# Performance work log

Hardware: AMD Instinct MI355X
Metric: run time of the kernel (lower is better)

The kernel has to match this reference:

```python
import jax, jax.numpy as jnp
import numpy as np

HEADS = 8
DIM = 64      # dim
DH = 64       # dim_head
DK = 24       # dim_k (== dim_head_k * heads, required by reshape in forward)
DHK = 3       # dim_head_k (also conv groups)


def setup_inputs() -> dict:
    key = jax.random.key(0)
    ks = jax.random.split(key, 10)
    b, h, w = 4, 128, 128
    return {
        "x_in": jax.random.normal(ks[0], (b, h, w, DIM), jnp.float32),
        "illu_fea_trans": jax.random.normal(ks[1], (b, h, w, DIM), jnp.float32),
        "illu_map_trans": jax.random.normal(ks[2], (b, h, w, DK), jnp.float32),
        # Linear weights stored as [in, out] (torch stores [out, in]; math y = x @ W_in_out)
        "Wq": jax.random.normal(ks[3], (DIM, HEADS * DH), jnp.float32) * 0.05,
        "Wk": jax.random.normal(ks[4], (DK, HEADS * DHK), jnp.float32) * 0.05,
        "Wv": jax.random.normal(ks[5], (DIM, HEADS * DH), jnp.float32) * 0.05,
        "rescale": jnp.ones((HEADS, 1, 1), jnp.float32),
        "Wp": jax.random.normal(ks[6], (HEADS * DHK, DK), jnp.float32) * 0.05,
        "bp": jax.random.normal(ks[7], (DK,), jnp.float32) * 0.05,
        # grouped conv weights, OIHW: [out=24, in/groups=8, 3, 3]
        "conv1_w": jax.random.normal(ks[8], (DK, DK // DHK, 3, 3), jnp.float32) * 0.05,
        "conv2_w": jax.random.normal(ks[9], (DK, DK // DHK, 3, 3), jnp.float32) * 0.05,
    }


def _gconv(x_nchw, w_oihw):
    return jax.lax.conv_general_dilated(
        x_nchw, w_oihw, window_strides=(1, 1), padding='SAME',
        feature_group_count=DHK,
        dimension_numbers=('NCHW', 'OIHW', 'NCHW'))


def reference(x_in, illu_fea_trans, illu_map_trans, Wq, Wk, Wv, rescale, Wp, bp, conv1_w, conv2_w):
    b, h, w, c = x_in.shape
    n = h * w
    # projections
    q = (x_in.reshape(b, n, c) @ Wq).reshape(b, n, HEADS, DH)
    k_inp = illu_map_trans.reshape(b, n, DK) @ Wk            # [b, n, heads*dhk]
    v = (illu_fea_trans.reshape(b, n, c) @ Wv).reshape(b, n, HEADS, DH)
    kh = k_inp.reshape(b, n, HEADS, DHK)
    q = q / (DIM ** 0.5)  # note: scaled by sqrt(dim), not sqrt(dim_head)
    # channel-wise cross-attention: attn over channel dims, contracting tokens n
    attn = jnp.einsum('bnhk,bnhd->bhkd', kh, q) * rescale[None]  # [b, heads, dhk, dh]
    attn = jax.nn.softmax(attn, axis=-1)
    out = jnp.einsum('bhkd,bnhd->bnkh', attn, v)             # [b, n, dhk, heads]
    out = out.reshape(b, n, DHK * HEADS) @ Wp + bp           # proj
    out = out.reshape(b, h, w, DK)
    # positional branch: two grouped 3x3 convs with exact GELU on k_inp
    kx = k_inp.reshape(b, h, w, DK).transpose(0, 3, 1, 2)    # NCHW
    y = _gconv(kx, conv1_w)
    y = jax.nn.gelu(y, approximate=False)
    y = _gconv(y, conv2_w)
    return out + y.transpose(0, 2, 3, 1)
```

## Files before the change

### kernel.cpp

```cpp
#include <hip/hip_runtime.h>
#include <math.h>

#define HEADS 8
#define DIM   64
#define DK    24
#define DHK   3
#define BB    4
#define HH    128
#define WW    128
#define NN    (HH*WW)
#define QSCALE 0.125f

__global__ __launch_bounds__(256) void s_reduce(
    const float* __restrict__ imap,
    const float* __restrict__ x,
    float* __restrict__ Sp_part)
{
    __shared__ float part[4*1536];
    const int tid = threadIdx.x;
    const int blk = blockIdx.x;
    const int b = blk >> 6, chunk = blk & 63;
    const int w = tid >> 6, lane = tid & 63;
    const int cq = lane & 15;
    const int ig = lane >> 4;

    const long tok0 = (long)b * NN + chunk * 256 + w * 64;
    const float* xp = x    + tok0 * 64 + cq * 4;
    const float* mp = imap + tok0 * 24 + ig * 6;

    float acc[6][4];
    #pragma unroll
    for (int r = 0; r < 6; ++r)
        #pragma unroll
        for (int q = 0; q < 4; ++q) acc[r][q] = 0.f;

    for (int t = 0; t < 64; ++t) {
        float4 xv = *(const float4*)(xp + t * 64);
        float2 m0 = *(const float2*)(mp + t * 24);
        float2 m1 = *(const float2*)(mp + t * 24 + 2);
        float2 m2 = *(const float2*)(mp + t * 24 + 4);
        float mm[6] = {m0.x, m0.y, m1.x, m1.y, m2.x, m2.y};
        #pragma unroll
        for (int r = 0; r < 6; ++r) {
            acc[r][0] += mm[r] * xv.x;
            acc[r][1] += mm[r] * xv.y;
            acc[r][2] += mm[r] * xv.z;
            acc[r][3] += mm[r] * xv.w;
        }
    }

    float* pp = part + w * 1536;
    #pragma unroll
    for (int r = 0; r < 6; ++r) {
        float4 v = {acc[r][0], acc[r][1], acc[r][2], acc[r][3]};
        *(float4*)(pp + (ig * 6 + r) * 64 + cq * 4) = v;
    }
    __syncthreads();

    for (int e = tid; e < 1536; e += 256)
        Sp_part[(long)blk * 1536 + e] =
            part[e] + part[1536 + e] + part[3072 + e] + part[4608 + e];
}

__global__ __launch_bounds__(256) void attn_fused(
    const float* __restrict__ Sp_part,
    const float* __restrict__ Wk,
    const float* __restrict__ Wq,
    const float* __restrict__ Wv,
    const float* __restrict__ rescale,
    const float* __restrict__ Wp,
    float* __restrict__ Pt)
{
    __shared__ float Sp_l[1536];
    __shared__ float S_l[1536];
    __shared__ float att[1536];
    __shared__ float M_l[1536];

    const int b = blockIdx.x, tid = threadIdx.x;

    {
        float s[6] = {0.f, 0.f, 0.f, 0.f, 0.f, 0.f};
        const float* p = Sp_part + (long)b * 64 * 1536;
        for (int c0 = 0; c0 < 64; c0 += 8) {
            float v[8][6];
            #pragma unroll
            for (int cc = 0; cc < 8; ++cc)
                #pragma unroll
                for (int k = 0; k < 6; ++k)
                    v[cc][k] = p[(long)(c0 + cc) * 1536 + tid + 256 * k];
            #pragma unroll
            for (int cc = 0; cc < 8; ++cc)
                #pragma unroll
                for (int k = 0; k < 6; ++k)
                    s[k] += v[cc][k];
        }
        #pragma unroll
        for (int k = 0; k < 6; ++k) Sp_l[tid + 256 * k] = s[k];
    }
    __syncthreads();

    for (int q = tid; q < 1536; q += 256) {
        int c = q & 63, j = q >> 6;
        float s = 0.f;
        #pragma unroll
        for (int i = 0; i < 24; ++i) s += Wk[i * 24 + j] * Sp_l[i * 64 + c];
        S_l[q] = s;
    }
    __syncthreads();

    for (int q = tid; q < 1536; q += 256) {
        int d = q & 63, ch = q >> 6;
        int h = ch / 3;
        const float* wq = Wq + h * 64 + d;
        const float* sr = S_l + ch * 64;
        float s = 0.f;
        for (int cc = 0; cc < 64; ++cc) s += sr[cc] * wq[cc * 512];
        att[q] = s * QSCALE * rescale[h];
    }
    __syncthreads();

    if (tid < 24) {
        float* row = att + tid * 64;
        float mx = row[0];
        for (int d = 1; d < 64; ++d) mx = fmaxf(mx, row[d]);
        float sum = 0.f;
        for (int d = 0; d < 64; ++d) { float e = expf(row[d] - mx); row[d] = e; sum += e; }
        float inv = 1.f / sum;
        for (int d = 0; d < 64; ++d) row[d] *= inv;
    }
    __syncthreads();

    for (int q = tid; q < 1536; q += 256) {
        int c = q & 63, ch = q >> 6;
        int h = ch / 3;
        const float* wv = Wv + c * 512 + h * 64;
        const float* ar = att + ch * 64;
        float s = 0.f;
        for (int d = 0; d < 64; ++d) s += ar[d] * wv[d];
        M_l[ch * 64 + c] = s;
    }
    __syncthreads();

    for (int q = tid; q < 1536; q += 256) {
        int c = q & 63, jo = q >> 6;
        float s = 0.f;
        #pragma unroll
        for (int k = 0; k < 3; ++k)
            #pragma unroll
            for (int h = 0; h < 8; ++h)
                s += M_l[(h * 3 + k) * 64 + c] * Wp[(k * 8 + h) * 24 + jo];
        Pt[b * 1536 + q] = s;
    }
}

__global__ __launch_bounds__(192, 2) void conv1_kproj_gelu(
    const float* __restrict__ imap, const float* __restrict__ Wk,
    const float* __restrict__ cw, float* __restrict__ y1)
{
    __shared__ __align__(16) float kbuf[100 * 28];

    const int tid = threadIdx.x;
    const int blk = blockIdx.x;
    const int b = blk >> 8, ti = (blk >> 4) & 15, tj = blk & 15;
    const int i0 = ti * 8, j0 = tj * 8;

    if (tid < 100) {
        const int pi = tid / 10, pj = tid % 10;
        const int gi = i0 + pi - 1, gj = j0 + pj - 1;
        float kv[24];
        #pragma unroll
        for (int j = 0; j < 24; ++j) kv[j] = 0.f;
        if (gi >= 0 && gi < HH && gj >= 0 && gj < WW) {
            const float4* m4 = (const float4*)(imap + (((long)b * HH + gi) * WW + gj) * 24);
            float m[24];
            #pragma unroll
            for (int i = 0; i < 6; ++i) {
                float4 v = m4[i];
                m[4*i+0]=v.x; m[4*i+1]=v.y; m[4*i+2]=v.z; m[4*i+3]=v.w;
            }
            for (int i = 0; i < 24; ++i) {
                float mi = m[i];
                #pragma unroll
                for (int j = 0; j < 24; ++j) kv[j] += mi * Wk[i * 24 + j];
            }
        }
        #pragma unroll
        for (int j = 0; j < 24; ++j) kbuf[tid * 28 + j] = kv[j];
    }
    __syncthreads();

    const int o = tid % 24, jj = tid / 24;
    const int g = o >> 3;

    float wr[8][9];
    {
        const float4* wp = (const float4*)(cw + o * 72);
        #pragma unroll
        for (int t = 0; t < 18; ++t) ((float4*)wr)[t] = wp[t];
    }

    float win[3][3][8];
    #define LROW(R, SLOT)                                                     \
    {                                                                         \
        const float* rp_ = kbuf + ((R) * 10 + jj) * 28 + g * 8;               \
        *(float4*)&win[SLOT][0][0] = *(const float4*)(rp_);                   \
        *(float4*)&win[SLOT][0][4] = *(const float4*)(rp_ + 4);               \
        *(float4*)&win[SLOT][1][0] = *(const float4*)(rp_ + 28);              \
        *(float4*)&win[SLOT][1][4] = *(const float4*)(rp_ + 32);              \
        *(float4*)&win[SLOT][2][0] = *(const float4*)(rp_ + 56);              \
        *(float4*)&win[SLOT][2][4] = *(const float4*)(rp_ + 60);              \
    }

    LROW(0, 0)
    LROW(1, 1)
    #pragma unroll
    for (int ii = 0; ii < 8; ++ii) {
        LROW(ii + 2, (ii + 2) % 3)
        float s = 0.f;
        #pragma unroll
        for (int di = 0; di < 3; ++di) {
            const int slot = (ii + di) % 3;
            #pragma unroll
            for (int dj = 0; dj < 3; ++dj)
                #pragma unroll
                for (int ic = 0; ic < 8; ++ic)
                    s += win[slot][dj][ic] * wr[ic][di * 3 + dj];
        }
        s = 0.5f * s * (1.f + erff(s * 0.70710678f));
        y1[((long)((b * HH + i0 + ii) * WW + j0)) * 24 + tid] = s;
    }
    #undef LROW
}

__global__ __launch_bounds__(192, 2) void conv2_proj(
    const float* __restrict__ y1, const float* __restrict__ fea,
    const float* __restrict__ cw2, const float* __restrict__ Pt,
    const float* __restrict__ bp, float* __restrict__ outp)
{
    const int tid = threadIdx.x;
    const int o = tid % 24, jj = tid / 24;
    const int blk = blockIdx.x;
    const int b = blk >> 8, ti = (blk >> 4) & 15, tj = blk & 15;
    const int i0 = ti * 8, j0 = tj * 8;
    const int g = o >> 3;

    float wr[8][9];
    {
        const float4* wp = (const float4*)(cw2 + o * 72);
        #pragma unroll
        for (int t = 0; t < 18; ++t) ((float4*)wr)[t] = wp[t];
    }
    const int gj0 = j0 + jj - 1;
    const bool cok0 = gj0 >= 0;
    const bool cok2 = (j0 + jj + 1) < WW;

    float acc[8];
    {
        const float bo = bp[o];
        #pragma unroll
        for (int ii = 0; ii < 8; ++ii) acc[ii] = bo;
        const float* PtRow = Pt + b * 1536 + o * 64;
        const float* feaB = fea + (((long)(b * HH + i0)) * WW + (j0 + jj)) * 64;
        for (int cq = 0; cq < 16; ++cq) {
            float4 p = *(const float4*)(PtRow + cq * 4);
            #pragma unroll
            for (int ii = 0; ii < 8; ++ii) {
                float4 f = *(const float4*)(feaB + (long)ii * WW * 64 + cq * 4);
                acc[ii] += f.x * p.x + f.y * p.y + f.z * p.z + f.w * p.w;
            }
        }
    }

    float win[3][3][8];
    #define LOADROW(GI, SLOT)                                                 \
    {                                                                         \
        const int gi_ = (GI);                                                 \
        const bool rok_ = (gi_ >= 0) & (gi_ < HH);                            \
        const float* rp_ = y1 + (long)b * NN * 24 + g * 8                     \
                         + ((long)gi_ * WW + gj0) * 24;                       \
        float4 z_ = {0.f,0.f,0.f,0.f};                                        \
        float4 a0_=z_, a1_=z_, b0_=z_, b1_=z_, c0_=z_, c1_=z_;                \
        if (rok_ & cok0) { a0_ = *(const float4*)(rp_);                       \
                           a1_ = *(const float4*)(rp_ + 4); }                 \
        if (rok_)        { b0_ = *(const float4*)(rp_ + 24);                  \
                           b1_ = *(const float4*)(rp_ + 28); }                \
        if (rok_ & cok2) { c0_ = *(const float4*)(rp_ + 48);                  \
                           c1_ = *(const float4*)(rp_ + 52); }                \
        *(float4*)&win[SLOT][0][0] = a0_; *(float4*)&win[SLOT][0][4] = a1_;   \
        *(float4*)&win[SLOT][1][0] = b0_; *(float4*)&win[SLOT][1][4] = b1_;   \
        *(float4*)&win[SLOT][2][0] = c0_; *(float4*)&win[SLOT][2][4] = c1_;   \
    }

    LOADROW(i0 - 1, 0)
    LOADROW(i0,     1)
    #pragma unroll
    for (int ii = 0; ii < 8; ++ii) {
        LOADROW(i0 + ii + 1, (ii + 2) % 3)
        float s = 0.f;
        #pragma unroll
        for (int di = 0; di < 3; ++di) {
            const int slot = (ii + di) % 3;
            #pragma unroll
            for (int dj = 0; dj < 3; ++dj)
                #pragma unroll
                for (int ic = 0; ic < 8; ++ic)
                    s += win[slot][dj][ic] * wr[ic][di * 3 + dj];
        }
        outp[((long)((b * HH + i0 + ii) * WW + j0)) * 24 + tid] = acc[ii] + s;
    }
    #undef LOADROW
}

extern "C" void kernel_launch(void* const* d_in, const int* in_sizes, int n_in,
                              void* d_out, int out_size, void* d_ws, size_t ws_size,
                              hipStream_t stream) {
    const float* x_in    = (const float*)d_in[0];
    const float* fea     = (const float*)d_in[1];
    const float* imap    = (const float*)d_in[2];
    const float* Wq      = (const float*)d_in[3];
    const float* Wk      = (const float*)d_in[4];
    const float* Wv      = (const float*)d_in[5];
    const float* rescale = (const float*)d_in[6];
    const float* Wp      = (const float*)d_in[7];
    const float* bp      = (const float*)d_in[8];
    const float* c1w     = (const float*)d_in[9];
    const float* c2w     = (const float*)d_in[10];
    float* out = (float*)d_out;

    float* ws      = (float*)d_ws;
    float* y1      = ws;
    float* Sp_part = ws + 1572864;
    float* Pt      = ws + 1966080;

    s_reduce<<<256, 256, 0, stream>>>(imap, x_in, Sp_part);
    attn_fused<<<4, 256, 0, stream>>>(Sp_part, Wk, Wq, Wv, rescale, Wp, Pt);
    conv1_kproj_gelu<<<BB * 256, 192, 0, stream>>>(imap, Wk, c1w, y1);
    conv2_proj<<<BB * 256, 192, 0, stream>>>(y1, fea, c2w, Pt, bp, out);
}
```

Baseline: 176.7 us.

## Fuse conv1 and conv2 into one kernel with haloed shared-memory tiles

Merges the k-projection+conv1+GELU kernel and the conv2+projection kernel into one kernel. Each block computes k_inp over a 12x12 halo tile, then conv1+GELU over a 10x10 tile into shared memory, then conv2 plus the attention projection for the 8x8 output. This removes the y1 global round trip and one launch, at the cost of halo recomputation (144 vs 100 k-projections, 100 vs 64 conv1 outputs per tile), more shared memory, and higher register pressure that may lower occupancy.

```diff
diff --git a/kernel.cpp b/kernel.cpp
--- a/kernel.cpp
+++ b/kernel.cpp
@@ -153,20 +153,25 @@
     }
 }
 
-__global__ __launch_bounds__(192, 2) void conv1_kproj_gelu(
+__global__ __launch_bounds__(192, 2) void conv_fused(
     const float* __restrict__ imap, const float* __restrict__ Wk,
-    const float* __restrict__ cw, float* __restrict__ y1)
+    const float* __restrict__ c1w,  const float* __restrict__ fea,
+    const float* __restrict__ c2w,  const float* __restrict__ Pt,
+    const float* __restrict__ bp,   float* __restrict__ outp)
 {
-    __shared__ __align__(16) float kbuf[100 * 28];
+    __shared__ __align__(16) float kbuf[144 * 28];
+    __shared__ __align__(16) float y1l[100 * 28];
 
     const int tid = threadIdx.x;
     const int blk = blockIdx.x;
     const int b = blk >> 8, ti = (blk >> 4) & 15, tj = blk & 15;
     const int i0 = ti * 8, j0 = tj * 8;
-
-    if (tid < 100) {
-        const int pi = tid / 10, pj = tid % 10;
-        const int gi = i0 + pi - 1, gj = j0 + pj - 1;
+    const int o = tid % 24, jj = tid / 24;
+    const int g = o >> 3;
+
+    if (tid < 144) {
+        const int pi = tid / 12, pj = tid % 12;
+        const int gi = i0 + pi - 2, gj = j0 + pj - 2;
         float kv[24];
         #pragma unroll
         for (int j = 0; j < 24; ++j) kv[j] = 0.f;
@@ -189,20 +194,81 @@
     }
     __syncthreads();
 
-    const int o = tid % 24, jj = tid / 24;
-    const int g = o >> 3;
+    {
+        float wr[8][9];
+        {
+            const float4* wp = (const float4*)(c1w + o * 72);
+            #pragma unroll
+            for (int t = 0; t < 18; ++t) ((float4*)wr)[t] = wp[t];
+        }
+        for (int task = tid; task < 240; task += 192) {
+            const int r = task / 24;
+            float wc[3][3][8];
+            #pragma unroll
+            for (int slot = 0; slot < 2; ++slot)
+                #pragma unroll
+                for (int di = 0; di < 3; ++di) {
+                    const float* p = kbuf + ((r + di) * 12 + slot) * 28 + g * 8;
+                    *(float4*)&wc[slot][di][0] = *(const float4*)(p);
+                    *(float4*)&wc[slot][di][4] = *(const float4*)(p + 4);
+                }
+            #pragma unroll
+            for (int c = 0; c < 10; ++c) {
+                const int s2 = (c + 2) % 3;
+                #pragma unroll
+                for (int di = 0; di < 3; ++di) {
+                    const float* p = kbuf + ((r + di) * 12 + (c + 2)) * 28 + g * 8;
+                    *(float4*)&wc[s2][di][0] = *(const float4*)(p);
+                    *(float4*)&wc[s2][di][4] = *(const float4*)(p + 4);
+                }
+                float s = 0.f;
+                #pragma unroll
+                for (int dj = 0; dj < 3; ++dj) {
+                    const int sl = (c + dj) % 3;
+                    #pragma unroll
+                    for (int di = 0; di < 3; ++di)
+                        #pragma unroll
+                        for (int ic = 0; ic < 8; ++ic)
+                            s += wc[sl][di][ic] * wr[ic][di * 3 + dj];
+                }
+                const int gi = i0 + r - 1, gj = j0 + c - 1;
+                float val = 0.f;
+                if (gi >= 0 && gi < HH && gj >= 0 && gj < WW)
+                    val = 0.5f * s * (1.f + erff(s * 0.70710678f));
+                y1l[(r * 10 + c) * 28 + o] = val;
+            }
+        }
+    }
+    __syncthreads();
 
     float wr[8][9];
     {
-        const float4* wp = (const float4*)(cw + o * 72);
+        const float4* wp = (const float4*)(c2w + o * 72);
         #pragma unroll
         for (int t = 0; t < 18; ++t) ((float4*)wr)[t] = wp[t];
+    }
+
+    float acc[8];
+    {
+        const float bo = bp[o];
+        #pragma unroll
+        for (int ii = 0; ii < 8; ++ii) acc[ii] = bo;
+        const float* PtRow = Pt + b * 1536 + o * 64;
+        const float* feaB = fea + (((long)(b * HH + i0)) * WW + (j0 + jj)) * 64;
+        for (int cq = 0; cq < 16; ++cq) {
+            float4 p = *(const float4*)(PtRow + cq * 4);
+            #pragma unroll
+            for (int ii = 0; ii < 8; ++ii) {
+                float4 f = *(const float4*)(feaB + (long)ii * WW * 64 + cq * 4);
+                acc[ii] += f.x * p.x + f.y * p.y + f.z * p.z + f.w * p.w;
+            }
+        }
     }
 
     float win[3][3][8];
     #define LROW(R, SLOT)                                                     \
     {                                                                         \
-        const float* rp_ = kbuf + ((R) * 10 + jj) * 28 + g * 8;               \
+        const float* rp_ = y1l + ((R) * 10 + jj) * 28 + g * 8;                \
         *(float4*)&win[SLOT][0][0] = *(const float4*)(rp_);                   \
         *(float4*)&win[SLOT][0][4] = *(const float4*)(rp_ + 4);               \
         *(float4*)&win[SLOT][1][0] = *(const float4*)(rp_ + 28);              \
@@ -226,89 +292,9 @@
                 for (int ic = 0; ic < 8; ++ic)
                     s += win[slot][dj][ic] * wr[ic][di * 3 + dj];
         }
-        s = 0.5f * s * (1.f + erff(s * 0.70710678f));
-        y1[((long)((b * HH + i0 + ii) * WW + j0)) * 24 + tid] = s;
+        outp[((long)((b * HH + i0 + ii) * WW + j0)) * 24 + tid] = acc[ii] + s;
     }
     #undef LROW
-}
-
-__global__ __launch_bounds__(192, 2) void conv2_proj(
-    const float* __restrict__ y1, const float* __restrict__ fea,
-    const float* __restrict__ cw2, const float* __restrict__ Pt,
-    const float* __restrict__ bp, float* __restrict__ outp)
-{
-    const int tid = threadIdx.x;
-    const int o = tid % 24, jj = tid / 24;
-    const int blk = blockIdx.x;
-    const int b = blk >> 8, ti = (blk >> 4) & 15, tj = blk & 15;
-    const int i0 = ti * 8, j0 = tj * 8;
-    const int g = o >> 3;
-
-    float wr[8][9];
-    {
-        const float4* wp = (const float4*)(cw2 + o * 72);
-        #pragma unroll
-        for (int t = 0; t < 18; ++t) ((float4*)wr)[t] = wp[t];
-    }
-    const int gj0 = j0 + jj - 1;
-    const bool cok0 = gj0 >= 0;
-    const bool cok2 = (j0 + jj + 1) < WW;
-
-    float acc[8];
-    {
-        const float bo = bp[o];
-        #pragma unroll
-        for (int ii = 0; ii < 8; ++ii) acc[ii] = bo;
-        const float* PtRow = Pt + b * 1536 + o * 64;
-        const float* feaB = fea + (((long)(b * HH + i0)) * WW + (j0 + jj)) * 64;
-        for (int cq = 0; cq < 16; ++cq) {
-            float4 p = *(const float4*)(PtRow + cq * 4);
-            #pragma unroll
-            for (int ii = 0; ii < 8; ++ii) {
-                float4 f = *(const float4*)(feaB + (long)ii * WW * 64 + cq * 4);
-                acc[ii] += f.x * p.x + f.y * p.y + f.z * p.z + f.w * p.w;
-            }
-        }
-    }
-
-    float win[3][3][8];
-    #define LOADROW(GI, SLOT)                                                 \
-    {                                                                         \
-        const int gi_ = (GI);                                                 \
-        const bool rok_ = (gi_ >= 0) & (gi_ < HH);                            \
-        const float* rp_ = y1 + (long)b * NN * 24 + g * 8                     \
-                         + ((long)gi_ * WW + gj0) * 24;                       \
-        float4 z_ = {0.f,0.f,0.f,0.f};                                        \
-        float4 a0_=z_, a1_=z_, b0_=z_, b1_=z_, c0_=z_, c1_=z_;                \
-        if (rok_ & cok0) { a0_ = *(const float4*)(rp_);                       \
-                           a1_ = *(const float4*)(rp_ + 4); }                 \
-        if (rok_)        { b0_ = *(const float4*)(rp_ + 24);                  \
-                           b1_ = *(const float4*)(rp_ + 28); }                \
-        if (rok_ & cok2) { c0_ = *(const float4*)(rp_ + 48);                  \
-                           c1_ = *(const float4*)(rp_ + 52); }                \
-        *(float4*)&win[SLOT][0][0] = a0_; *(float4*)&win[SLOT][0][4] = a1_;   \
-        *(float4*)&win[SLOT][1][0] = b0_; *(float4*)&win[SLOT][1][4] = b1_;   \
-        *(float4*)&win[SLOT][2][0] = c0_; *(float4*)&win[SLOT][2][4] = c1_;   \
-    }
-
-    LOADROW(i0 - 1, 0)
-    LOADROW(i0,     1)
-    #pragma unroll
-    for (int ii = 0; ii < 8; ++ii) {
-        LOADROW(i0 + ii + 1, (ii + 2) % 3)
-        float s = 0.f;
-        #pragma unroll
-        for (int di = 0; di < 3; ++di) {
-            const int slot = (ii + di) % 3;
-            #pragma unroll
-            for (int dj = 0; dj < 3; ++dj)
-                #pragma unroll
-                for (int ic = 0; ic < 8; ++ic)
-                    s += win[slot][dj][ic] * wr[ic][di * 3 + dj];
-        }
-        outp[((long)((b * HH + i0 + ii) * WW + j0)) * 24 + tid] = acc[ii] + s;
-    }
-    #undef LOADROW
 }
 
 extern "C" void kernel_launch(void* const* d_in, const int* in_sizes, int n_in,
@@ -328,12 +314,10 @@
     float* out = (float*)d_out;
 
     float* ws      = (float*)d_ws;
-    float* y1      = ws;
-    float* Sp_part = ws + 1572864;
-    float* Pt      = ws + 1966080;
+    float* Sp_part = ws;
+    float* Pt      = ws + 393216;
 
     s_reduce<<<256, 256, 0, stream>>>(imap, x_in, Sp_part);
     attn_fused<<<4, 256, 0, stream>>>(Sp_part, Wk, Wq, Wv, rescale, Wp, Pt);
-    conv1_kproj_gelu<<<BB * 256, 192, 0, stream>>>(imap, Wk, c1w, y1);
-    conv2_proj<<<BB * 256, 192, 0, stream>>>(y1, fea, c2w, Pt, bp, out);
+    conv_fused<<<BB * 256, 192, 0, stream>>>(imap, Wk, c1w, fea, c2w, Pt, bp, out);
 }
```

Result: no change. 174.1 us (-1.5%).
